# Performance work log

Hardware: AMD Instinct MI355X
Metric: run time of the kernel (lower is better)

The kernel has to match this reference:

```python
import jax, jax.numpy as jnp
import numpy as np

N_NODES = 100000
N_EDGES = 1250000
IN_FEATS = 64
OUT_FEATS = 64


def setup_inputs() -> dict:
    key = jax.random.key(0)
    k_h, k_src, k_dst, k_w, k_b = jax.random.split(key, 5)
    h = jax.random.normal(k_h, (N_NODES, IN_FEATS), dtype=jnp.float32)
    src = jax.random.randint(k_src, (N_EDGES,), 0, N_NODES, dtype=jnp.int64)
    dst = jax.random.randint(k_dst, (N_EDGES,), 0, N_NODES, dtype=jnp.int64)
    # torch nn.Linear: weight [out, in], bias [out], uniform(-stdv, stdv)
    stdv = 1.0 / np.sqrt(IN_FEATS)
    W = jax.random.uniform(k_w, (OUT_FEATS, IN_FEATS), dtype=jnp.float32, minval=-stdv, maxval=stdv)
    b = jax.random.uniform(k_b, (OUT_FEATS,), dtype=jnp.float32, minval=-stdv, maxval=stdv)
    return {"h": h, "src": src, "dst": dst, "W": W, "b": b}


def reference(h, src, dst, W, b):
    # update_all(copy_src, sum): ah[v] = sum over edges (u->v) of h[u]
    msgs = h[src]                                   # [E, in] irregular gather
    ah = jax.ops.segment_sum(msgs, dst, num_segments=N_NODES)  # [N, in] scatter-add
    out = ah @ W.T + b                              # linear
    return jax.nn.relu(out)
```

## Files before the change

kernel.cpp:

```cpp
#include <hip/hip_runtime.h>

#define N_NODES 100000
#define N_EDGES 1250000
#define FEATS 64

#define NPB   128
#define NBUCK ((N_NODES + NPB - 1) / NPB)
#define CAP   2304
#define TILE  4096
#define NTILES ((N_EDGES + TILE - 1) / TILE)
#define PK_BLOCKS ((N_NODES + 255) / 256)

typedef unsigned short ushort8 __attribute__((ext_vector_type(8)));

__device__ __forceinline__ float bf2f(unsigned short u) {
    return __uint_as_float(((unsigned int)u) << 16);
}
__device__ __forceinline__ unsigned short f2bf(float f) {
    unsigned int x = __float_as_uint(f);
    unsigned int lsb = (x >> 16) & 1u;
    x += 0x7fffu + lsb;
    return (unsigned short)(x >> 16);
}


__global__ __launch_bounds__(256) void pack_kernel(
        const float* __restrict__ h,
        const float* __restrict__ W,
        unsigned short* __restrict__ hwb) {
    const int n = blockIdx.x * 256 + threadIdx.x;
    if (n >= N_NODES) return;

    float hr[FEATS];
    const float4* hp = (const float4*)(h + (size_t)n * FEATS);
#pragma unroll
    for (int k4 = 0; k4 < 16; ++k4) {
        float4 v = hp[k4];
        hr[k4 * 4 + 0] = v.x; hr[k4 * 4 + 1] = v.y;
        hr[k4 * 4 + 2] = v.z; hr[k4 * 4 + 3] = v.w;
    }

    for (int ob = 0; ob < 8; ++ob) {
        ushort8 u;
#pragma unroll
        for (int oi = 0; oi < 8; ++oi) {
            const float* wrow = W + (size_t)(ob * 8 + oi) * FEATS;
            float acc = 0.f;
#pragma unroll
            for (int k4 = 0; k4 < 16; ++k4) {
                float4 w = *(const float4*)(wrow + k4 * 4);
                acc = fmaf(hr[k4 * 4 + 0], w.x, acc);
                acc = fmaf(hr[k4 * 4 + 1], w.y, acc);
                acc = fmaf(hr[k4 * 4 + 2], w.z, acc);
                acc = fmaf(hr[k4 * 4 + 3], w.w, acc);
            }
            u[oi] = f2bf(acc);
        }
        *(ushort8*)(hwb + (size_t)n * FEATS + ob * 8) = u;
    }
}

__global__ __launch_bounds__(256) void bin_kernel(
        const int* __restrict__ src,
        const int* __restrict__ dst,
        int* __restrict__ cursor,
        int* __restrict__ pairs) {
    __shared__ int hist[NBUCK];
    __shared__ int base[NBUCK];
    const int t  = threadIdx.x;
    const int e0 = blockIdx.x * TILE + t * 16;
    const bool full = (blockIdx.x + 1) * TILE <= N_EDGES;

    for (int i = t; i < NBUCK; i += 256) hist[i] = 0;
    __syncthreads();

    int d[16], lr[16];
    if (full) {
#pragma unroll
        for (int q = 0; q < 4; ++q) {
            int4 v = *(const int4*)(dst + e0 + q * 4);
            d[q * 4 + 0] = v.x; d[q * 4 + 1] = v.y;
            d[q * 4 + 2] = v.z; d[q * 4 + 3] = v.w;
        }
#pragma unroll
        for (int j = 0; j < 16; ++j) lr[j] = atomicAdd(&hist[d[j] >> 7], 1);
    } else {
#pragma unroll
        for (int j = 0; j < 16; ++j) {
            if (e0 + j < N_EDGES) {
                d[j]  = dst[e0 + j];
                lr[j] = atomicAdd(&hist[d[j] >> 7], 1);
            }
        }
    }
    __syncthreads();

    for (int i = t; i < NBUCK; i += 256)
        base[i] = hist[i] ? atomicAdd(&cursor[i], hist[i]) : 0;
    __syncthreads();

    if (full) {
        int s[16];
#pragma unroll
        for (int q = 0; q < 4; ++q) {
            int4 v = *(const int4*)(src + e0 + q * 4);
            s[q * 4 + 0] = v.x; s[q * 4 + 1] = v.y;
            s[q * 4 + 2] = v.z; s[q * 4 + 3] = v.w;
        }
#pragma unroll
        for (int j = 0; j < 16; ++j) {
            int bk  = d[j] >> 7;
            int rel = base[bk] + lr[j];
            if (rel < CAP)
                pairs[(size_t)bk * CAP + rel] = (s[j] << 7) | (d[j] & (NPB - 1));
        }
    } else {
#pragma unroll
        for (int j = 0; j < 16; ++j) {
            if (e0 + j < N_EDGES) {
                int bk  = d[j] >> 7;
                int rel = base[bk] + lr[j];
                if (rel < CAP)
                    pairs[(size_t)bk * CAP + rel] =
                        (src[e0 + j] << 7) | (d[j] & (NPB - 1));
            }
        }
    }
}

__global__ __launch_bounds__(256) void agg_kernel(
        const unsigned short* __restrict__ hwb,
        const int* __restrict__ pairs,
        const int* __restrict__ cursor,
        const float* __restrict__ bias,
        float* __restrict__ out) {
    __shared__ int ssrc[CAP];
    __shared__ int lcnt[NPB];
    __shared__ int loff[NPB + 1];
    __shared__ int lcur[NPB];

    const int tid  = threadIdx.x;
    const int lane = tid & 63;
    const int wv   = tid >> 6;
    const int g    = lane >> 3;
    const int li   = lane & 7;
    const int fo   = li * 8;

    const float4 bv0 = *(const float4*)(bias + fo);
    const float4 bv1 = *(const float4*)(bias + fo + 4);

    const int b = blockIdx.x;
    int size = cursor[b];
    if (size > CAP) size = CAP;
    const int* bp = pairs + (size_t)b * CAP;

    if (tid < NPB) lcnt[tid] = 0;
    __syncthreads();
    for (int i = tid; i < size; i += 256) atomicAdd(&lcnt[bp[i] & (NPB - 1)], 1);
    __syncthreads();
    if (tid < NPB) lcur[tid] = lcnt[tid];
    __syncthreads();
    for (int off = 1; off < NPB; off <<= 1) {
        int y = 0;
        if (tid < NPB && tid >= off) y = lcur[tid - off];
        __syncthreads();
        if (tid < NPB) lcur[tid] += y;
        __syncthreads();
    }
    if (tid < NPB) loff[tid + 1] = lcur[tid];
    if (tid == 0) loff[0] = 0;
    __syncthreads();
    if (tid < NPB) lcur[tid] = loff[tid];
    __syncthreads();
    for (int i = tid; i < size; i += 256) {
        int p = bp[i];
        int r = atomicAdd(&lcur[p & (NPB - 1)], 1);
        ssrc[r] = p >> 7;
    }
    __syncthreads();

#pragma unroll
    for (int pass = 0; pass < 4; ++pass) {
        const int ln  = pass * 32 + wv * 8 + g;
        const int beg = loff[ln];
        const int m   = loff[ln + 1] - beg;

        float acc0[8], acc1[8];
#pragma unroll
        for (int i = 0; i < 8; ++i) { acc0[i] = 0.f; acc1[i] = 0.f; }

        for (int base = 0; __any(base < m); base += 8) {
#pragma unroll
            for (int t = 0; t < 8; t += 2) {
                const int i0 = base + t, i1 = base + t + 1;
                int r0 = (i0 < m) ? ssrc[beg + i0] : 0;
                int r1 = (i1 < m) ? ssrc[beg + i1] : 0;
                if (i0 < m) {
                    ushort8 u = *(const ushort8*)(hwb + (size_t)r0 * FEATS + fo);
#pragma unroll
                    for (int i = 0; i < 8; ++i) acc0[i] += bf2f(u[i]);
                }
                if (i1 < m) {
                    ushort8 u = *(const ushort8*)(hwb + (size_t)r1 * FEATS + fo);
#pragma unroll
                    for (int i = 0; i < 8; ++i) acc1[i] += bf2f(u[i]);
                }
            }
        }

        const int nn = b * NPB + ln;
        if (nn < N_NODES) {
            float4 o0, o1;
            o0.x = fmaxf(acc0[0] + acc1[0] + bv0.x, 0.f);
            o0.y = fmaxf(acc0[1] + acc1[1] + bv0.y, 0.f);
            o0.z = fmaxf(acc0[2] + acc1[2] + bv0.z, 0.f);
            o0.w = fmaxf(acc0[3] + acc1[3] + bv0.w, 0.f);
            o1.x = fmaxf(acc0[4] + acc1[4] + bv1.x, 0.f);
            o1.y = fmaxf(acc0[5] + acc1[5] + bv1.y, 0.f);
            o1.z = fmaxf(acc0[6] + acc1[6] + bv1.z, 0.f);
            o1.w = fmaxf(acc0[7] + acc1[7] + bv1.w, 0.f);
            float* op = out + (size_t)nn * FEATS + fo;
            *(float4*)op       = o0;
            *(float4*)(op + 4) = o1;
        }
    }
}

extern "C" void kernel_launch(void* const* d_in, const int* in_sizes, int n_in,
                              void* d_out, int out_size, void* d_ws, size_t ws_size,
                              hipStream_t stream) {
    const float* h   = (const float*)d_in[0];
    const int*   src = (const int*)d_in[1];
    const int*   dst = (const int*)d_in[2];
    const float* W   = (const float*)d_in[3];
    const float* b   = (const float*)d_in[4];
    float* out = (float*)d_out;

    int* cursor = (int*)d_ws;
    int* pairs  = cursor + 1024;
    unsigned short* hwb = (unsigned short*)(pairs + (size_t)NBUCK * CAP);

    hipMemsetAsync(cursor, 0, 1024 * sizeof(int), stream);
    bin_kernel<<<NTILES, 256, 0, stream>>>(src, dst, cursor, pairs);
    pack_kernel<<<PK_BLOCKS, 256, 0, stream>>>(h, W, hwb);
    agg_kernel<<<NBUCK, 256, 0, stream>>>(hwb, pairs, cursor, b, out);
}
```

Baseline: 193.3 us.

## Restructure linear pack kernel to stage node rows in LDS, lane-per-output

The pack kernel now loads a 64-node tile of h into shared memory with coalesced float4 loads. Each lane of a wave computes one output feature for 16 nodes, reading W rows per lane and broadcasting h rows from LDS, then writes bf16 results one element per lane. This replaces the per-thread approach, which held a whole 64-float row in registers and issued strided, uncoalesced global loads. In exchange, W rows are re-read from cache inside the node loop, and output stores become 2-byte scalar writes instead of 16-byte vectors.

```diff
diff --git a/kernel.cpp b/kernel.cpp
--- a/kernel.cpp
+++ b/kernel.cpp
@@ -9,7 +9,8 @@
 #define CAP   2304
 #define TILE  4096
 #define NTILES ((N_EDGES + TILE - 1) / TILE)
-#define PK_BLOCKS ((N_NODES + 255) / 256)
+#define PK_NPB 64
+#define PK_BLOCKS ((N_NODES + PK_NPB - 1) / PK_NPB)
 
 typedef unsigned short ushort8 __attribute__((ext_vector_type(8)));
 
@@ -28,35 +29,44 @@
         const float* __restrict__ h,
         const float* __restrict__ W,
         unsigned short* __restrict__ hwb) {
-    const int n = blockIdx.x * 256 + threadIdx.x;
-    if (n >= N_NODES) return;
-
-    float hr[FEATS];
-    const float4* hp = (const float4*)(h + (size_t)n * FEATS);
-#pragma unroll
-    for (int k4 = 0; k4 < 16; ++k4) {
-        float4 v = hp[k4];
-        hr[k4 * 4 + 0] = v.x; hr[k4 * 4 + 1] = v.y;
-        hr[k4 * 4 + 2] = v.z; hr[k4 * 4 + 3] = v.w;
-    }
-
-    for (int ob = 0; ob < 8; ++ob) {
-        ushort8 u;
-#pragma unroll
-        for (int oi = 0; oi < 8; ++oi) {
-            const float* wrow = W + (size_t)(ob * 8 + oi) * FEATS;
-            float acc = 0.f;
-#pragma unroll
-            for (int k4 = 0; k4 < 16; ++k4) {
-                float4 w = *(const float4*)(wrow + k4 * 4);
-                acc = fmaf(hr[k4 * 4 + 0], w.x, acc);
-                acc = fmaf(hr[k4 * 4 + 1], w.y, acc);
-                acc = fmaf(hr[k4 * 4 + 2], w.z, acc);
-                acc = fmaf(hr[k4 * 4 + 3], w.w, acc);
-            }
-            u[oi] = f2bf(acc);
-        }
-        *(ushort8*)(hwb + (size_t)n * FEATS + ob * 8) = u;
+    __shared__ float sh[PK_NPB][68];
+
+    const int tid  = threadIdx.x;
+    const int lane = tid & 63;
+    const int wv   = tid >> 6;
+    const int n0   = blockIdx.x * PK_NPB;
+
+#pragma unroll
+    for (int it = 0; it < 4; ++it) {
+        const int pos = it * 256 + tid;
+        const int row = pos >> 4;
+        const int c4  = pos & 15;
+        if (n0 + row < N_NODES) {
+            float4 v = *(const float4*)(h + (size_t)(n0 + row) * FEATS + c4 * 4);
+            *(float4*)&sh[row][c4 * 4] = v;
+        }
+    }
+    __syncthreads();
+
+    const float* wrow = W + (size_t)lane * FEATS;
+
+#pragma unroll 2
+    for (int q = 0; q < 16; ++q) {
+        const int nl = wv * 16 + q;
+        const int nn = n0 + nl;
+        if (nn >= N_NODES) break;
+        const float4* ar = (const float4*)&sh[nl][0];
+        float acc = 0.f;
+#pragma unroll
+        for (int k4 = 0; k4 < 16; ++k4) {
+            float4 w4 = *(const float4*)(wrow + k4 * 4);
+            float4 r  = ar[k4];
+            acc = fmaf(r.x, w4.x, acc);
+            acc = fmaf(r.y, w4.y, acc);
+            acc = fmaf(r.z, w4.z, acc);
+            acc = fmaf(r.w, w4.w, acc);
+        }
+        hwb[(size_t)nn * FEATS + lane] = f2bf(acc);
     }
 }
 
```

After: 192.7 us. About the same (-0.3%).
